# Kernel optimization log

Measured on AMD Instinct MI355X. Metric: run time of the kernel, lower is better.

Reference implementation:

```python
import jax, jax.numpy as jnp
import numpy as np

B, S, D = 2, 2048, 1024
FC = 4096
H = 16
EPS = 1e-5


def _layer_norm(x, g, b):
    mu = jnp.mean(x, axis=-1, keepdims=True)
    var = jnp.var(x, axis=-1, keepdims=True)
    return (x - mu) * jax.lax.rsqrt(var + EPS) * g + b


def setup_inputs() -> dict:
    key = jax.random.key(0)
    ks = jax.random.split(key, 8)
    s = 0.02
    return {
        "x": jax.random.normal(ks[0], (B, S, D), dtype=jnp.float32),
        "ln1_g": jnp.ones((D,), jnp.float32),
        "ln1_b": jnp.zeros((D,), jnp.float32),
        "w_qkv": jax.random.normal(ks[1], (D, 3 * D), dtype=jnp.float32) * s,
        "b_qkv": jnp.zeros((3 * D,), jnp.float32),
        "ln2_g": jnp.ones((D,), jnp.float32),
        "ln2_b": jnp.zeros((D,), jnp.float32),
        "w1": jax.random.normal(ks[2], (D, FC), dtype=jnp.float32) * s,
        "b1": jnp.zeros((FC,), jnp.float32),
        "w2": jax.random.normal(ks[3], (FC, D), dtype=jnp.float32) * s,
        "b2": jnp.zeros((D,), jnp.float32),
    }


def reference(x, ln1_g, ln1_b, w_qkv, b_qkv, ln2_g, ln2_b, w1, b1, w2, b2):
    # pre-LN attention block
    h = _layer_norm(x, ln1_g, ln1_b)
    qkv = h @ w_qkv + b_qkv                       # [B,S,3D]
    q, k, v = jnp.split(qkv, 3, axis=-1)
    hd = D // H
    q = q.reshape(B, S, H, hd)
    k = k.reshape(B, S, H, hd)
    v = v.reshape(B, S, H, hd)
    scale = 1.0 / jnp.sqrt(jnp.float32(hd))
    scores = jnp.einsum("bqhd,bkhd->bhqk", q, k) * scale
    a = jax.nn.softmax(scores, axis=-1)           # [B,H,S,S]
    attn = jnp.einsum("bhqk,bkhd->bqhd", a, v).reshape(B, S, D)
    attn = attn + x
    # MLP block
    h2 = _layer_norm(attn, ln2_g, ln2_b)
    m = jax.nn.relu(h2 @ w1 + b1)
    out = m @ w2 + b2 + attn
    return out
```

## Files before the change

### kernel.cpp

```cpp
#include <hip/hip_runtime.h>
#include <stdint.h>

typedef __bf16 bf16x8 __attribute__((ext_vector_type(8)));
typedef __bf16 bf16x4 __attribute__((ext_vector_type(4)));
typedef float f32x4 __attribute__((ext_vector_type(4)));

__device__ __forceinline__ void g2l16(const void* gp, void* lp) {
  __builtin_amdgcn_global_load_lds(
      (__attribute__((address_space(1))) void*)const_cast<void*>(gp),
      (__attribute__((address_space(3))) void*)lp, 16, 0, 0);
}

__global__ __launch_bounds__(256) void ln_bf16(
    const float* __restrict__ in, const float* __restrict__ g,
    const float* __restrict__ b, __bf16* __restrict__ out) {
  int row = blockIdx.x;
  int t = threadIdx.x;
  const float4* rp = (const float4*)(in + (size_t)row * 1024);
  float4 v = rp[t];
  float s = v.x + v.y + v.z + v.w;
  float ss = v.x * v.x + v.y * v.y + v.z * v.z + v.w * v.w;
#pragma unroll
  for (int o = 32; o; o >>= 1) {
    s += __shfl_down(s, o, 64);
    ss += __shfl_down(ss, o, 64);
  }
  __shared__ float red[8];
  int w = t >> 6;
  if ((t & 63) == 0) { red[w] = s; red[4 + w] = ss; }
  __syncthreads();
  float S1 = red[0] + red[1] + red[2] + red[3];
  float S2 = red[4] + red[5] + red[6] + red[7];
  float mu = S1 * (1.0f / 1024.0f);
  float var = S2 * (1.0f / 1024.0f) - mu * mu;
  float rstd = rsqrtf(var + 1e-5f);
  int c = t * 4;
  float4 gv = ((const float4*)g)[t];
  float4 bv = ((const float4*)b)[t];
  __bf16* op = out + (size_t)row * 1024 + c;
  op[0] = (__bf16)((v.x - mu) * rstd * gv.x + bv.x);
  op[1] = (__bf16)((v.y - mu) * rstd * gv.y + bv.y);
  op[2] = (__bf16)((v.z - mu) * rstd * gv.z + bv.z);
  op[3] = (__bf16)((v.w - mu) * rstd * gv.w + bv.w);
}

__global__ __launch_bounds__(256) void tcast(const float* __restrict__ in,
                                             __bf16* __restrict__ out, int R,
                                             int C) {
  __shared__ float t[32][33];
  int c0 = blockIdx.x * 32, r0 = blockIdx.y * 32;
  int tx = threadIdx.x & 31, ty = threadIdx.x >> 5;
#pragma unroll
  for (int i = 0; i < 4; i++)
    t[ty + i * 8][tx] = in[(size_t)(r0 + ty + i * 8) * C + c0 + tx];
  __syncthreads();
#pragma unroll
  for (int i = 0; i < 4; i++)
    out[(size_t)(c0 + ty + i * 8) * R + r0 + tx] = (__bf16)t[tx][ty + i * 8];
}

__global__ __launch_bounds__(256) void vtrans(const __bf16* __restrict__ qkv,
                                              __bf16* __restrict__ vT) {
  __shared__ __bf16 t[64][72];
  int bh = blockIdx.y, s0 = blockIdx.x * 64;
  int tid = threadIdx.x;
  int b = bh >> 4, h = bh & 15;
  int r = tid >> 2, c = (tid & 3) * 16;
  const __bf16* src =
      qkv + (size_t)(b * 2048 + s0 + r) * 3072 + 2048 + h * 64 + c;
  *(bf16x8*)&t[r][c] = *(const bf16x8*)src;
  *(bf16x8*)&t[r][c + 8] = *(const bf16x8*)(src + 8);
  __syncthreads();
  int d = tid >> 2;
  int cs = (tid & 3) * 16;
  __bf16 tmp[16] __attribute__((aligned(16)));
#pragma unroll
  for (int u = 0; u < 16; u++) tmp[u] = t[cs + u][d];
  __bf16* dst = vT + (size_t)(bh * 64 + d) * 2048 + s0 + cs;
  *(bf16x8*)dst = *(bf16x8*)&tmp[0];
  *(bf16x8*)(dst + 8) = *(bf16x8*)&tmp[8];
}

template <int EPI>
__global__ __launch_bounds__(256) void gemm_bt(
    const __bf16* __restrict__ A, const __bf16* __restrict__ BT,
    const float* __restrict__ bias, const float* __restrict__ res,
    void* __restrict__ out, int M, int N, int K) {
  __shared__ __bf16 As[128 * 32];
  __shared__ __bf16 Bs[128 * 32];
  int tid = threadIdx.x;
  int m0 = blockIdx.y * 128, n0 = blockIdx.x * 128;
  int lane = tid & 63, w = tid >> 6;
  int wm = (w >> 1) * 64, wn = (w & 1) * 64;
  int quad = lane >> 4, lm = lane & 15;

  int kc = K / (int)gridDim.z;
  int kBeg = (int)blockIdx.z * kc;
  int kEnd = kBeg + kc;

  f32x4 acc[4][4] = {};

  int sr = tid >> 2;
  int sc = (((tid & 3) - ((tid >> 3) & 3)) & 3) * 8;
  const __bf16* aRow = A + (size_t)(m0 + sr) * K + sc;
  const __bf16* bRow = BT + (size_t)(n0 + sr) * K + sc;
  size_t step64a = (size_t)64 * K;

  for (int k0 = kBeg; k0 < kEnd; k0 += 32) {
    g2l16(aRow + k0, &As[tid * 8]);
    g2l16(aRow + step64a + k0, &As[2048 + tid * 8]);
    g2l16(bRow + k0, &Bs[tid * 8]);
    g2l16(bRow + step64a + k0, &Bs[2048 + tid * 8]);
    __syncthreads();
    bf16x8 af[4], bv[4];
#pragma unroll
    for (int i = 0; i < 4; i++) {
      int ar = wm + i * 16 + lm;
      af[i] = *(const bf16x8*)&As[ar * 32 + ((quad + (ar >> 1)) & 3) * 8];
    }
#pragma unroll
    for (int j = 0; j < 4; j++) {
      int br = wn + j * 16 + lm;
      bv[j] = *(const bf16x8*)&Bs[br * 32 + ((quad + (br >> 1)) & 3) * 8];
    }
#pragma unroll
    for (int i = 0; i < 4; i++)
#pragma unroll
      for (int j = 0; j < 4; j++)
        acc[i][j] =
            __builtin_amdgcn_mfma_f32_16x16x32_bf16(af[i], bv[j], acc[i][j], 0, 0, 0);
    __syncthreads();
  }

#pragma unroll
  for (int i = 0; i < 4; i++)
#pragma unroll
    for (int j = 0; j < 4; j++) {
      int rg0 = m0 + wm + i * 16 + quad * 4;
      int cg = n0 + wn + j * 16 + lm;
      float bi = (EPI == 3) ? 0.0f : bias[cg];
#pragma unroll
      for (int r = 0; r < 4; r++) {
        int rg = rg0 + r;
        float v = acc[i][j][r] + bi;
        if (EPI == 1) v = fmaxf(v, 0.0f);
        if (EPI == 2) {
          ((float*)out)[(size_t)rg * N + cg] = v + res[(size_t)rg * N + cg];
        } else if (EPI == 3) {
          ((__bf16*)out)[(size_t)blockIdx.z * M * N + (size_t)rg * N + cg] =
              (__bf16)v;
        } else {
          ((__bf16*)out)[(size_t)rg * N + cg] = (__bf16)v;
        }
      }
    }
}

__global__ __launch_bounds__(256) void reduce_mlp2(
    const __bf16* __restrict__ part, const float* __restrict__ bias,
    const float* __restrict__ res, float* __restrict__ out) {
  size_t i = ((size_t)blockIdx.x * 256 + threadIdx.x) * 8;
  const size_t plane = (size_t)4096 * 1024;
  bf16x8 p0 = *(const bf16x8*)(part + i);
  bf16x8 p1 = *(const bf16x8*)(part + plane + i);
  bf16x8 p2 = *(const bf16x8*)(part + 2 * plane + i);
  bf16x8 p3 = *(const bf16x8*)(part + 3 * plane + i);
  int n0 = (int)(i & 1023);
  float4 b0 = *(const float4*)(bias + n0);
  float4 b1 = *(const float4*)(bias + n0 + 4);
  float4 r0 = *(const float4*)(res + i);
  float4 r1 = *(const float4*)(res + i + 4);
  float4 o0, o1;
  o0.x = (float)p0[0] + (float)p1[0] + (float)p2[0] + (float)p3[0] + b0.x + r0.x;
  o0.y = (float)p0[1] + (float)p1[1] + (float)p2[1] + (float)p3[1] + b0.y + r0.y;
  o0.z = (float)p0[2] + (float)p1[2] + (float)p2[2] + (float)p3[2] + b0.z + r0.z;
  o0.w = (float)p0[3] + (float)p1[3] + (float)p2[3] + (float)p3[3] + b0.w + r0.w;
  o1.x = (float)p0[4] + (float)p1[4] + (float)p2[4] + (float)p3[4] + b1.x + r1.x;
  o1.y = (float)p0[5] + (float)p1[5] + (float)p2[5] + (float)p3[5] + b1.y + r1.y;
  o1.z = (float)p0[6] + (float)p1[6] + (float)p2[6] + (float)p3[6] + b1.z + r1.z;
  o1.w = (float)p0[7] + (float)p1[7] + (float)p2[7] + (float)p3[7] + b1.w + r1.w;
  *(float4*)(out + i) = o0;
  *(float4*)(out + i + 4) = o1;
}

__global__ __launch_bounds__(512) void attn_kernel(
    const __bf16* __restrict__ qkv, const __bf16* __restrict__ vT,
    const float* __restrict__ x, float* __restrict__ attnres) {
  int qb = blockIdx.x, h = blockIdx.y, b = blockIdx.z;
  int tid = threadIdx.x, lane = tid & 63, w = tid >> 6;
  int quad = lane >> 4, lm = lane & 15;
  int q0 = qb * 128;

  __shared__ __bf16 Qs[128 * 64];
  __shared__ __bf16 Ks[64 * 64];
  __shared__ __bf16 Vs[64 * 64];
  __shared__ __bf16 Ps[8][16 * 72];

  const __bf16* qbase = qkv + (size_t)(b * 2048) * 3072 + h * 64;
  const __bf16* kbase = qkv + (size_t)(b * 2048) * 3072 + 1024 + h * 64;
  const __bf16* vbase = vT + (size_t)((b * 16 + h) * 64) * 2048;

  int sr = tid >> 3;
  int sc = (((tid & 7) - sr) & 7) * 8;

  g2l16(qbase + (size_t)(q0 + sr) * 3072 + sc, &Qs[tid * 8]);
  g2l16(qbase + (size_t)(q0 + 64 + sr) * 3072 + sc, &Qs[4096 + tid * 8]);
  __syncthreads();

  int qrow = w * 16 + lm;
  bf16x8 qf0 = *(const bf16x8*)&Qs[qrow * 64 + ((quad + qrow) & 7) * 8];
  bf16x8 qf1 = *(const bf16x8*)&Qs[qrow * 64 + ((4 + quad + qrow) & 7) * 8];

  f32x4 acc_o[4] = {};
  float rs = 0.0f;
  const float cexp = 0.18033688f;

  for (int s0 = 0; s0 < 2048; s0 += 64) {
    g2l16(kbase + (size_t)(s0 + sr) * 3072 + sc, &Ks[tid * 8]);
    g2l16(vbase + (size_t)sr * 2048 + s0 + sc, &Vs[tid * 8]);
    __syncthreads();

#pragma unroll
    for (int j = 0; j < 4; j++) {
      int krow = j * 16 + lm;
      bf16x8 kf0 = *(const bf16x8*)&Ks[krow * 64 + ((quad + krow) & 7) * 8];
      bf16x8 kf1 = *(const bf16x8*)&Ks[krow * 64 + ((4 + quad + krow) & 7) * 8];
      f32x4 z = {0.0f, 0.0f, 0.0f, 0.0f};
      z = __builtin_amdgcn_mfma_f32_16x16x32_bf16(kf0, qf0, z, 0, 0, 0);
      z = __builtin_amdgcn_mfma_f32_16x16x32_bf16(kf1, qf1, z, 0, 0, 0);
      bf16x4 pw;
#pragma unroll
      for (int rr = 0; rr < 4; rr++) {
        float e = exp2f(z[rr] * cexp);
        rs += e;
        pw[rr] = (__bf16)e;
      }
      *(bf16x4*)&Ps[w][lm * 72 + j * 16 + quad * 4] = pw;
    }
    bf16x8 pf0 = *(const bf16x8*)&Ps[w][lm * 72 + quad * 8];
    bf16x8 pf1 = *(const bf16x8*)&Ps[w][lm * 72 + 32 + quad * 8];
#pragma unroll
    for (int jd = 0; jd < 4; jd++) {
      int vrow = jd * 16 + lm;
      bf16x8 vf0 = *(const bf16x8*)&Vs[vrow * 64 + ((quad + vrow) & 7) * 8];
      bf16x8 vf1 = *(const bf16x8*)&Vs[vrow * 64 + ((4 + quad + vrow) & 7) * 8];
      acc_o[jd] =
          __builtin_amdgcn_mfma_f32_16x16x32_bf16(vf0, pf0, acc_o[jd], 0, 0, 0);
      acc_o[jd] =
          __builtin_amdgcn_mfma_f32_16x16x32_bf16(vf1, pf1, acc_o[jd], 0, 0, 0);
    }
    __syncthreads();
  }

  rs += __shfl_xor(rs, 16);
  rs += __shfl_xor(rs, 32);
  float inv = 1.0f / rs;

  int qg = q0 + w * 16 + lm;
  const float* xrow = x + ((size_t)(b * 2048 + qg)) * 1024 + h * 64;
  float* orow = attnres + ((size_t)(b * 2048 + qg)) * 1024 + h * 64;
#pragma unroll
  for (int jd = 0; jd < 4; jd++) {
    int d0 = jd * 16 + quad * 4;
    float4 xv = *(const float4*)(xrow + d0);
    float4 ov;
    ov.x = acc_o[jd][0] * inv + xv.x;
    ov.y = acc_o[jd][1] * inv + xv.y;
    ov.z = acc_o[jd][2] * inv + xv.z;
    ov.w = acc_o[jd][3] * inv + xv.w;
    *(float4*)(orow + d0) = ov;
  }
}

extern "C" void kernel_launch(void* const* d_in, const int* in_sizes, int n_in,
                              void* d_out, int out_size, void* d_ws,
                              size_t ws_size, hipStream_t stream) {
  const float* x = (const float*)d_in[0];
  const float* ln1_g = (const float*)d_in[1];
  const float* ln1_b = (const float*)d_in[2];
  const float* w_qkv = (const float*)d_in[3];
  const float* b_qkv = (const float*)d_in[4];
  const float* ln2_g = (const float*)d_in[5];
  const float* ln2_b = (const float*)d_in[6];
  const float* w1 = (const float*)d_in[7];
  const float* b1 = (const float*)d_in[8];
  const float* w2 = (const float*)d_in[9];
  const float* b2 = (const float*)d_in[10];
  float* out = (float*)d_out;

  char* ws = (char*)d_ws;
  size_t o = 0;
  float* attnres = (float*)(ws + o);  o += (size_t)4096 * 1024 * 4;
  __bf16* mmid = (__bf16*)(ws + o);   o += (size_t)4096 * 4096 * 2;
  __bf16* w2T = (__bf16*)(ws + o);    o += (size_t)1024 * 4096 * 2;
  size_t base2 = o;
  __bf16* h1 = (__bf16*)(ws + o);     o += (size_t)4096 * 1024 * 2;
  __bf16* wqkvT = (__bf16*)(ws + o);  o += (size_t)3072 * 1024 * 2;
  __bf16* w1T = (__bf16*)(ws + o);    o += (size_t)4096 * 1024 * 2;
  __bf16* qkvb = (__bf16*)(ws + o);   o += (size_t)4096 * 3072 * 2;
  __bf16* vTb = (__bf16*)(ws + o);    o += (size_t)32 * 64 * 2048 * 2;
  __bf16* h2 = (__bf16*)(ws + o);     o += (size_t)4096 * 1024 * 2;
  __bf16* partials = (__bf16*)(ws + base2);

  tcast<<<dim3(96, 32), 256, 0, stream>>>(w_qkv, wqkvT, 1024, 3072);
  tcast<<<dim3(128, 32), 256, 0, stream>>>(w1, w1T, 1024, 4096);
  tcast<<<dim3(32, 128), 256, 0, stream>>>(w2, w2T, 4096, 1024);

  ln_bf16<<<4096, 256, 0, stream>>>(x, ln1_g, ln1_b, h1);
  gemm_bt<0><<<dim3(24, 32), 256, 0, stream>>>(h1, wqkvT, b_qkv, nullptr, qkvb,
                                               4096, 3072, 1024);
  vtrans<<<dim3(32, 32), 256, 0, stream>>>(qkvb, vTb);
  attn_kernel<<<dim3(16, 16, 2), 512, 0, stream>>>(qkvb, vTb, x, attnres);
  ln_bf16<<<4096, 256, 0, stream>>>(attnres, ln2_g, ln2_b, h2);
  gemm_bt<1><<<dim3(32, 32), 256, 0, stream>>>(h2, w1T, b1, nullptr, mmid, 4096,
                                               4096, 1024);
  gemm_bt<3><<<dim3(8, 32, 4), 256, 0, stream>>>(mmid, w2T, nullptr, nullptr,
                                                 partials, 4096, 1024, 4096);
  reduce_mlp2<<<2048, 256, 0, stream>>>(partials, b2, attnres, out);
}
```

Before: 361.4 us.

## Software-pipeline attention loop with double-buffered K and triple-buffered V

The attention kernel now prefetches the next K/V tiles into rotating LDS buffers while computing the current tile. The P·V product is deferred by one iteration so it overlaps with the next QK^T, and each iteration needs one barrier instead of two. This hides global-to-LDS load latency behind MFMA work but uses more LDS per block, which may lower occupancy.

New measurement: 362.6 us. About the same (+0.3%).

```diff
diff --git a/kernel.cpp b/kernel.cpp
--- a/kernel.cpp
+++ b/kernel.cpp
@@ -192,8 +192,8 @@
   int q0 = qb * 128;
 
   __shared__ __bf16 Qs[128 * 64];
-  __shared__ __bf16 Ks[64 * 64];
-  __shared__ __bf16 Vs[64 * 64];
+  __shared__ __bf16 Kbuf[2][64 * 64];
+  __shared__ __bf16 Vbuf[3][64 * 64];
   __shared__ __bf16 Ps[8][16 * 72];
 
   const __bf16* qbase = qkv + (size_t)(b * 2048) * 3072 + h * 64;
@@ -205,6 +205,8 @@
 
   g2l16(qbase + (size_t)(q0 + sr) * 3072 + sc, &Qs[tid * 8]);
   g2l16(qbase + (size_t)(q0 + 64 + sr) * 3072 + sc, &Qs[4096 + tid * 8]);
+  g2l16(kbase + (size_t)sr * 3072 + sc, &Kbuf[0][tid * 8]);
+  g2l16(vbase + (size_t)sr * 2048 + sc, &Vbuf[0][tid * 8]);
   __syncthreads();
 
   int qrow = w * 16 + lm;
@@ -215,11 +217,23 @@
   float rs = 0.0f;
   const float cexp = 0.18033688f;
 
-  for (int s0 = 0; s0 < 2048; s0 += 64) {
-    g2l16(kbase + (size_t)(s0 + sr) * 3072 + sc, &Ks[tid * 8]);
-    g2l16(vbase + (size_t)sr * 2048 + s0 + sc, &Vs[tid * 8]);
-    __syncthreads();
-
+  const __bf16* kpre = kbase + (size_t)(64 + sr) * 3072 + sc;
+  const __bf16* vpre = vbase + (size_t)sr * 2048 + 64 + sc;
+  __bf16* pv = Vbuf[2];
+  __bf16* cv = Vbuf[0];
+  __bf16* nv = Vbuf[1];
+  int kcur = 0;
+
+  for (int t = 0; t < 32; ++t) {
+    bf16x8 pf0 = *(const bf16x8*)&Ps[w][lm * 72 + quad * 8];
+    bf16x8 pf1 = *(const bf16x8*)&Ps[w][lm * 72 + 32 + quad * 8];
+    if (t < 31) {
+      g2l16(kpre, &Kbuf[kcur ^ 1][tid * 8]);
+      g2l16(vpre, &nv[tid * 8]);
+      kpre += (size_t)64 * 3072;
+      vpre += 64;
+    }
+    const __bf16* Ks = Kbuf[kcur];
 #pragma unroll
     for (int j = 0; j < 4; j++) {
       int krow = j * 16 + lm;
@@ -237,19 +251,37 @@
       }
       *(bf16x4*)&Ps[w][lm * 72 + j * 16 + quad * 4] = pw;
     }
+    if (t > 0) {
+#pragma unroll
+      for (int jd = 0; jd < 4; jd++) {
+        int vrow = jd * 16 + lm;
+        bf16x8 vf0 = *(const bf16x8*)&pv[vrow * 64 + ((quad + vrow) & 7) * 8];
+        bf16x8 vf1 =
+            *(const bf16x8*)&pv[vrow * 64 + ((4 + quad + vrow) & 7) * 8];
+        acc_o[jd] = __builtin_amdgcn_mfma_f32_16x16x32_bf16(vf0, pf0,
+                                                            acc_o[jd], 0, 0, 0);
+        acc_o[jd] = __builtin_amdgcn_mfma_f32_16x16x32_bf16(vf1, pf1,
+                                                            acc_o[jd], 0, 0, 0);
+      }
+    }
+    __bf16* tmp = pv; pv = cv; cv = nv; nv = tmp;
+    kcur ^= 1;
+    __syncthreads();
+  }
+
+  {
     bf16x8 pf0 = *(const bf16x8*)&Ps[w][lm * 72 + quad * 8];
     bf16x8 pf1 = *(const bf16x8*)&Ps[w][lm * 72 + 32 + quad * 8];
 #pragma unroll
     for (int jd = 0; jd < 4; jd++) {
       int vrow = jd * 16 + lm;
-      bf16x8 vf0 = *(const bf16x8*)&Vs[vrow * 64 + ((quad + vrow) & 7) * 8];
-      bf16x8 vf1 = *(const bf16x8*)&Vs[vrow * 64 + ((4 + quad + vrow) & 7) * 8];
-      acc_o[jd] =
-          __builtin_amdgcn_mfma_f32_16x16x32_bf16(vf0, pf0, acc_o[jd], 0, 0, 0);
-      acc_o[jd] =
-          __builtin_amdgcn_mfma_f32_16x16x32_bf16(vf1, pf1, acc_o[jd], 0, 0, 0);
-    }
-    __syncthreads();
+      bf16x8 vf0 = *(const bf16x8*)&pv[vrow * 64 + ((quad + vrow) & 7) * 8];
+      bf16x8 vf1 = *(const bf16x8*)&pv[vrow * 64 + ((4 + quad + vrow) & 7) * 8];
+      acc_o[jd] = __builtin_amdgcn_mfma_f32_16x16x32_bf16(vf0, pf0, acc_o[jd],
+                                                          0, 0, 0);
+      acc_o[jd] = __builtin_amdgcn_mfma_f32_16x16x32_bf16(vf1, pf1, acc_o[jd],
+                                                          0, 0, 0);
+    }
   }
 
   rs += __shfl_xor(rs, 16);
```
